# Performance work log

Hardware: AMD Instinct MI355X
Metric: run time of the kernel (lower is better)

Reference implementation:

```python
import jax, jax.numpy as jnp
import numpy as np

B, L, A, D = 16, 1024, 512, 1024


def setup_inputs() -> dict:
    key = jax.random.key(0)
    ks = jax.random.split(key, 12)
    s = 1.0 / np.sqrt(D)
    s2 = 1.0 / np.sqrt(2 * D)
    return {
        "text_features": jax.random.normal(ks[0], (B, L, D), jnp.float32),
        "audio_features": jax.random.normal(ks[1], (B, A, D), jnp.float32),
        "Wt1": jax.random.uniform(ks[2], (D, D), jnp.float32, -s, s),
        "bt1": jax.random.uniform(ks[3], (D,), jnp.float32, -s, s),
        "Wa1": jax.random.uniform(ks[4], (D, D), jnp.float32, -s, s),
        "w_att1": jax.random.uniform(ks[5], (2 * D,), jnp.float32, -s2, s2),
        "b_att1": jax.random.uniform(ks[6], (), jnp.float32, -s2, s2),
        "Wt2": jax.random.uniform(ks[7], (D, D), jnp.float32, -s, s),
        "Wa2": jax.random.uniform(ks[8], (D, D), jnp.float32, -s, s),
        "ba2": jax.random.uniform(ks[9], (D,), jnp.float32, -s, s),
        "w_att2": jax.random.uniform(ks[10], (2 * D,), jnp.float32, -s2, s2),
        "b_att2": jax.random.uniform(ks[11], (), jnp.float32, -s2, s2),
    }


def reference(text_features, audio_features, Wt1, bt1, Wa1, w_att1, b_att1,
              Wt2, Wa2, ba2, w_att2, b_att2):
    # Additive co-attention. tanh(cat([u_i, v_j])) = cat([tanh(u_i), tanh(v_j)]),
    # so the post-tanh linear score decomposes into an outer sum — exact same math
    # as the naive repeat/cat/tanh/linear, without the (B,L,A,2D) intermediate.
    d = Wt1.shape[0]
    # --- attention over audio regions ---
    u1 = jnp.tanh(jnp.einsum('bld,ed->ble', text_features, Wt1) + bt1)   # (B,L,D)
    v1 = jnp.tanh(jnp.einsum('bad,ed->bae', audio_features, Wa1))        # (B,A,D)
    scores1 = (u1 @ w_att1[:d])[:, :, None] + (v1 @ w_att1[d:])[:, None, :] + b_att1  # (B,L,A)
    audio_att = jax.nn.softmax(scores1, axis=-1)
    att_audio_features = jnp.einsum('bla,bad->bld', audio_att, audio_features)  # (B,L,D)
    # --- attention over text positions (self.args.max_seq_len == L) ---
    u2 = jnp.tanh(jnp.einsum('bld,ed->ble', att_audio_features, Wa2) + ba2)  # (B,L,D)
    v2 = jnp.tanh(jnp.einsum('bkd,ed->bke', text_features, Wt2))             # (B,L,D)
    scores2 = (u2 @ w_att2[:d])[:, :, None] + (v2 @ w_att2[d:])[:, None, :] + b_att2  # (B,L,L)
    textual_att = jax.nn.softmax(scores2, axis=-1)
    att_text_features = jnp.einsum('blk,bkd->bld', textual_att, text_features)
    return (att_text_features, att_audio_features)
```

## Files before the change

kernel.cpp:

```cpp
#include <hip/hip_runtime.h>

typedef unsigned short u16;
typedef float f32x4 __attribute__((ext_vector_type(4)));
typedef int   i32x4 __attribute__((ext_vector_type(4)));
typedef u16   u16x8 __attribute__((ext_vector_type(8)));

#define LDS_STRIDE 40

__device__ __forceinline__ u16 f2bf(float f) {
  unsigned u = __float_as_uint(f);
  u += 0x7FFFu + ((u >> 16) & 1u);
  return (u16)(u >> 16);
}

__device__ __forceinline__ float tanh_fast(float x) {
  float e = __expf(2.0f * x);
  return 1.0f - 2.0f / (e + 1.0f);
}

__device__ __forceinline__ void mfma_bf16(f32x4& acc, i32x4 a, i32x4 b) {
  asm("v_mfma_f32_16x16x32_bf16 %0, %1, %2, %0" : "+v"(acc) : "v"(a), "v"(b));
}

__global__ __launch_bounds__(256) void cast_all_kernel(
    const float* __restrict__ text, const float* __restrict__ audio,
    const float* __restrict__ w2, const float* __restrict__ w1,
    u16* __restrict__ tb, u16* __restrict__ ab,
    u16* __restrict__ w2b, u16* __restrict__ w1b) {
  const int NTOT = 3407872;
  int stride = gridDim.x * 256;
  for (int i = blockIdx.x * 256 + threadIdx.x; i < NTOT; i += stride) {
    const float* src; u16* dst; int j;
    if (i < 2097152)      { src = text;  dst = tb;  j = i; }
    else if (i < 3145728) { src = audio; dst = ab;  j = i - 2097152; }
    else if (i < 3276800) { src = w2;    dst = w2b; j = i - 3145728; }
    else                  { src = w1;    dst = w1b; j = i - 3276800; }
    const float4* s = (const float4*)src;
    float4 a = s[2 * j], b = s[2 * j + 1];
    u16x8 o;
    o[0] = f2bf(a.x); o[1] = f2bf(a.y); o[2] = f2bf(a.z); o[3] = f2bf(a.w);
    o[4] = f2bf(b.x); o[5] = f2bf(b.y); o[6] = f2bf(b.z); o[7] = f2bf(b.w);
    *(u16x8*)(dst + (size_t)8 * j) = o;
  }
}

__global__ __launch_bounds__(256) void score_kernel(
    const u16* __restrict__ Xa, const u16* __restrict__ Wa,
    const float* __restrict__ wva, float* __restrict__ sva,
    const u16* __restrict__ Xt, const u16* __restrict__ Wt,
    const float* __restrict__ wvt, float* __restrict__ svt) {
  __shared__ u16 At[128 * LDS_STRIDE];
  __shared__ u16 Bt[128 * LDS_STRIDE];

  int bx = blockIdx.x;
  const u16 *X, *W; const float* wv; float* svout; int mt, split, M;
  if (bx < 256) { X = Xa; W = Wa; wv = wva; svout = sva; M = 8192;  mt = bx >> 2; split = bx & 3; }
  else { bx -= 256; X = Xt; W = Wt; wv = wvt; svout = svt; M = 16384; mt = bx >> 2; split = bx & 3; }

  const int t = threadIdx.x;
  const int wid = t >> 6, lane = t & 63;
  const int wm = wid >> 1, wn = wid & 1;
  const int lane15 = lane & 15, lg = lane >> 4;
  const size_t m_base = (size_t)mt * 128;

  float rs[4][4];
  #pragma unroll
  for (int mi = 0; mi < 4; ++mi)
    #pragma unroll
    for (int r = 0; r < 4; ++r) rs[mi][r] = 0.f;

  const int li0 = t, li1 = 256 + t;
  const int ar0 = li0 >> 2, ac0 = (li0 & 3) * 8;
  const int ar1 = li1 >> 2, ac1 = (li1 & 3) * 8;

  for (int nt = 0; nt < 2; ++nt) {
    const int n0 = split * 256 + nt * 128;

    f32x4 acc[4][4];
    #pragma unroll
    for (int mi = 0; mi < 4; ++mi)
      #pragma unroll
      for (int ni = 0; ni < 4; ++ni)
        acc[mi][ni] = (f32x4){0.f, 0.f, 0.f, 0.f};

    const u16* Xb = X + m_base * 1024;
    const u16* Wb = W + (size_t)n0 * 1024;

    i32x4 ra0 = *(const i32x4*)(Xb + (size_t)ar0 * 1024 + ac0);
    i32x4 ra1 = *(const i32x4*)(Xb + (size_t)ar1 * 1024 + ac1);
    i32x4 rb0 = *(const i32x4*)(Wb + (size_t)ar0 * 1024 + ac0);
    i32x4 rb1 = *(const i32x4*)(Wb + (size_t)ar1 * 1024 + ac1);

    for (int kt = 0; kt < 32; ++kt) {
      __syncthreads();
      *(i32x4*)(At + li0 * 8 / 8 * 0 + ar0 * LDS_STRIDE + ac0) = ra0;
      *(i32x4*)(At + ar1 * LDS_STRIDE + ac1) = ra1;
      *(i32x4*)(Bt + ar0 * LDS_STRIDE + ac0) = rb0;
      *(i32x4*)(Bt + ar1 * LDS_STRIDE + ac1) = rb1;
      __syncthreads();
      if (kt < 31) {
        const int k1 = (kt + 1) * 32;
        ra0 = *(const i32x4*)(Xb + (size_t)ar0 * 1024 + k1 + ac0);
        ra1 = *(const i32x4*)(Xb + (size_t)ar1 * 1024 + k1 + ac1);
        rb0 = *(const i32x4*)(Wb + (size_t)ar0 * 1024 + k1 + ac0);
        rb1 = *(const i32x4*)(Wb + (size_t)ar1 * 1024 + k1 + ac1);
      }
      i32x4 af[4], bfr[4];
      #pragma unroll
      for (int mi = 0; mi < 4; ++mi)
        af[mi] = *(const i32x4*)(At + (wm * 64 + mi * 16 + lane15) * LDS_STRIDE + lg * 8);
      #pragma unroll
      for (int ni = 0; ni < 4; ++ni)
        bfr[ni] = *(const i32x4*)(Bt + (wn * 64 + ni * 16 + lane15) * LDS_STRIDE + lg * 8);
      #pragma unroll
      for (int mi = 0; mi < 4; ++mi)
        #pragma unroll
        for (int ni = 0; ni < 4; ++ni)
          mfma_bf16(acc[mi][ni], af[mi], bfr[ni]);
    }

    float wvn[4];
    #pragma unroll
    for (int ni = 0; ni < 4; ++ni) wvn[ni] = wv[n0 + wn * 64 + ni * 16 + lane15];
    #pragma unroll
    for (int mi = 0; mi < 4; ++mi)
      #pragma unroll
      for (int ni = 0; ni < 4; ++ni)
        #pragma unroll
        for (int r = 0; r < 4; ++r)
          rs[mi][r] += tanh_fast(acc[mi][ni][r]) * wvn[ni];
  }

  __syncthreads();
  float* sred = (float*)At;
  #pragma unroll
  for (int mi = 0; mi < 4; ++mi)
    #pragma unroll
    for (int r = 0; r < 4; ++r) {
      float v = rs[mi][r];
      v += __shfl_xor(v, 1);
      v += __shfl_xor(v, 2);
      v += __shfl_xor(v, 4);
      v += __shfl_xor(v, 8);
      if (lane15 == 0) sred[wn * 128 + wm * 64 + mi * 16 + lg * 4 + r] = v;
    }
  __syncthreads();
  if (t < 128) svout[(size_t)split * M + m_base + t] = sred[t] + sred[128 + t];
}

__global__ __launch_bounds__(256) void softq_bcast_kernel(
    const float* __restrict__ xA, const float* __restrict__ svA,
    const float* __restrict__ xT, const float* __restrict__ svT,
    float* __restrict__ out) {
  int bx = blockIdx.x;
  int stage = bx >> 8;
  int b = (bx >> 4) & 15, dch = bx & 15;
  int Acnt = stage ? 1024 : 512;
  int M = stage ? 16384 : 8192;
  const float* x = stage ? xT : xA;
  const float* svp = stage ? svT : svA;
  int rowbase = b * Acnt;

  __shared__ float p[1024];
  __shared__ float red[256];
  __shared__ float chunk[64];
  int t = threadIdx.x;

  float mloc = -1e30f;
  for (int a = t; a < Acnt; a += 256) {
    float v = svp[rowbase + a] + svp[M + rowbase + a] +
              svp[2 * M + rowbase + a] + svp[3 * M + rowbase + a];
    p[a] = v;
    mloc = fmaxf(mloc, v);
  }
  #pragma unroll
  for (int off = 32; off; off >>= 1) mloc = fmaxf(mloc, __shfl_xor(mloc, off));
  if ((t & 63) == 0) red[t >> 6] = mloc;
  __syncthreads();
  float mx = fmaxf(fmaxf(red[0], red[1]), fmaxf(red[2], red[3]));

  float sloc = 0.f;
  for (int a = t; a < Acnt; a += 256) {
    float e = __expf(p[a] - mx);
    p[a] = e;
    sloc += e;
  }
  #pragma unroll
  for (int off = 32; off; off >>= 1) sloc += __shfl_xor(sloc, off);
  __syncthreads();
  if ((t & 63) == 0) red[t >> 6] = sloc;
  __syncthreads();
  float inv = 1.0f / (red[0] + red[1] + red[2] + red[3]);

  int dl = t & 63, ag = t >> 6;
  const float* xb = x + (size_t)rowbase * 1024 + dch * 64 + dl;
  float acc = 0.f;
  #pragma unroll 4
  for (int a = ag; a < Acnt; a += 4) acc += p[a] * xb[(size_t)a * 1024];
  __syncthreads();
  red[t] = acc;
  __syncthreads();
  if (t < 64) {
    float tot = red[t] + red[t + 64] + red[t + 128] + red[t + 192];
    chunk[t] = tot * inv;
  }
  __syncthreads();

  size_t base4 = ((stage ? (size_t)0 : (size_t)16777216) +
                  (size_t)b * 1048576 + (size_t)dch * 64) >> 2;
  float4* o4 = (float4*)out;
  float4 v = ((float4*)chunk)[t & 15];
  int q = t & 15;
  #pragma unroll 4
  for (int l = t >> 4; l < 1024; l += 16)
    o4[base4 + (size_t)l * 256 + q] = v;
}

extern "C" void kernel_launch(void* const* d_in, const int* in_sizes, int n_in,
                              void* d_out, int out_size, void* d_ws, size_t ws_size,
                              hipStream_t stream) {
  const float* text  = (const float*)d_in[0];
  const float* audio = (const float*)d_in[1];
  const float* Wa1   = (const float*)d_in[4];
  const float* watt1 = (const float*)d_in[5];
  const float* Wt2   = (const float*)d_in[7];
  const float* watt2 = (const float*)d_in[10];

  char* ws = (char*)d_ws;
  u16*   tb  = (u16*)(ws);
  u16*   ab  = (u16*)(ws + 33554432);
  u16*   w2b = (u16*)(ws + 50331648);
  u16*   w1b = (u16*)(ws + 52428800);
  float* sv2 = (float*)(ws + 54525952);
  float* sv1 = (float*)(ws + 54788096);

  cast_all_kernel<<<2048, 256, 0, stream>>>(text, audio, Wt2, Wa1, tb, ab, w2b, w1b);

  score_kernel<<<768, 256, 0, stream>>>(ab, w1b, watt1 + 1024, sv1,
                                        tb, w2b, watt2 + 1024, sv2);

  softq_bcast_kernel<<<512, 256, 0, stream>>>(audio, sv1, text, sv2, (float*)d_out);
}
```

Measured before the change: 349.3 us.

## Fuse activation bf16 cast into score GEMM, swizzle LDS, nontemporal broadcast stores

The separate cast pass over text and audio activations is removed. The score GEMM now loads fp32 activations directly and converts them to bf16 in registers with packed cvt before writing to LDS, so a full bf16 copy of the inputs is no longer written and re-read. LDS padding is replaced by an XOR swizzle, the block-to-tile mapping is remapped so blocks sharing a weight slice run together, the softmax reduction loop is unrolled further, and output broadcast stores use nontemporal hints. In exchange, the GEMM A-operand loads become twice as wide in bytes, and each activation tile is cast once per n-tile and per split instead of once overall.

```diff
diff --git a/kernel.cpp b/kernel.cpp
--- a/kernel.cpp
+++ b/kernel.cpp
@@ -5,7 +5,7 @@
 typedef int   i32x4 __attribute__((ext_vector_type(4)));
 typedef u16   u16x8 __attribute__((ext_vector_type(8)));
 
-#define LDS_STRIDE 40
+#define SWZ(i) ((i) ^ ((((i) >> 6) & 3) << 3))
 
 __device__ __forceinline__ u16 f2bf(float f) {
   unsigned u = __float_as_uint(f);
@@ -13,6 +13,12 @@
   return (u16)(u >> 16);
 }
 
+__device__ __forceinline__ int cvt_pk_bf16(float lo, float hi) {
+  int r;
+  asm("v_cvt_pk_bf16_f32 %0, %1, %2" : "=v"(r) : "v"(lo), "v"(hi));
+  return r;
+}
+
 __device__ __forceinline__ float tanh_fast(float x) {
   float e = __expf(2.0f * x);
   return 1.0f - 2.0f / (e + 1.0f);
@@ -22,40 +28,39 @@
   asm("v_mfma_f32_16x16x32_bf16 %0, %1, %2, %0" : "+v"(acc) : "v"(a), "v"(b));
 }
 
-__global__ __launch_bounds__(256) void cast_all_kernel(
-    const float* __restrict__ text, const float* __restrict__ audio,
+__global__ __launch_bounds__(256) void wcast_kernel(
     const float* __restrict__ w2, const float* __restrict__ w1,
-    u16* __restrict__ tb, u16* __restrict__ ab,
     u16* __restrict__ w2b, u16* __restrict__ w1b) {
-  const int NTOT = 3407872;
-  int stride = gridDim.x * 256;
-  for (int i = blockIdx.x * 256 + threadIdx.x; i < NTOT; i += stride) {
-    const float* src; u16* dst; int j;
-    if (i < 2097152)      { src = text;  dst = tb;  j = i; }
-    else if (i < 3145728) { src = audio; dst = ab;  j = i - 2097152; }
-    else if (i < 3276800) { src = w2;    dst = w2b; j = i - 3145728; }
-    else                  { src = w1;    dst = w1b; j = i - 3276800; }
-    const float4* s = (const float4*)src;
-    float4 a = s[2 * j], b = s[2 * j + 1];
-    u16x8 o;
-    o[0] = f2bf(a.x); o[1] = f2bf(a.y); o[2] = f2bf(a.z); o[3] = f2bf(a.w);
-    o[4] = f2bf(b.x); o[5] = f2bf(b.y); o[6] = f2bf(b.z); o[7] = f2bf(b.w);
-    *(u16x8*)(dst + (size_t)8 * j) = o;
-  }
+  int i = blockIdx.x * 256 + threadIdx.x;
+  const float* src; u16* dst; int j;
+  if (i < 131072) { src = w2; dst = w2b; j = i; }
+  else            { src = w1; dst = w1b; j = i - 131072; }
+  const float4* s = (const float4*)src;
+  float4 a = s[2 * j], b = s[2 * j + 1];
+  u16x8 o;
+  o[0] = f2bf(a.x); o[1] = f2bf(a.y); o[2] = f2bf(a.z); o[3] = f2bf(a.w);
+  o[4] = f2bf(b.x); o[5] = f2bf(b.y); o[6] = f2bf(b.z); o[7] = f2bf(b.w);
+  *(u16x8*)(dst + (size_t)8 * j) = o;
 }
 
 __global__ __launch_bounds__(256) void score_kernel(
-    const u16* __restrict__ Xa, const u16* __restrict__ Wa,
+    const float* __restrict__ audio, const u16* __restrict__ w1b,
     const float* __restrict__ wva, float* __restrict__ sva,
-    const u16* __restrict__ Xt, const u16* __restrict__ Wt,
+    const float* __restrict__ text, const u16* __restrict__ w2b,
     const float* __restrict__ wvt, float* __restrict__ svt) {
-  __shared__ u16 At[128 * LDS_STRIDE];
-  __shared__ u16 Bt[128 * LDS_STRIDE];
+  __shared__ u16 At[128 * 32];
+  __shared__ u16 Bt[128 * 32];
 
   int bx = blockIdx.x;
-  const u16 *X, *W; const float* wv; float* svout; int mt, split, M;
-  if (bx < 256) { X = Xa; W = Wa; wv = wva; svout = sva; M = 8192;  mt = bx >> 2; split = bx & 3; }
-  else { bx -= 256; X = Xt; W = Wt; wv = wvt; svout = svt; M = 16384; mt = bx >> 2; split = bx & 3; }
+  const float* Xf; const u16* Wb_; const float* wv; float* svout; int mt, split, M;
+  if (bx < 256) {
+    Xf = audio; Wb_ = w1b; wv = wva; svout = sva; M = 8192;
+    mt = (bx & 7) * 8 + (bx >> 5); split = (bx >> 3) & 3;
+  } else {
+    int x = bx - 256;
+    Xf = text; Wb_ = w2b; wv = wvt; svout = svt; M = 16384;
+    mt = (x & 7) * 16 + (x >> 5); split = (x >> 3) & 3;
+  }
 
   const int t = threadIdx.x;
   const int wid = t >> 6, lane = t & 63;
@@ -69,9 +74,11 @@
     #pragma unroll
     for (int r = 0; r < 4; ++r) rs[mi][r] = 0.f;
 
-  const int li0 = t, li1 = 256 + t;
-  const int ar0 = li0 >> 2, ac0 = (li0 & 3) * 8;
-  const int ar1 = li1 >> 2, ac1 = (li1 & 3) * 8;
+  const int ar0 = t >> 2,        ac0 = (t & 3) * 8;
+  const int ar1 = (256 + t) >> 2, ac1 = (t & 3) * 8;
+  const int wiA0 = SWZ(ar0 * 32 + ac0), wiA1 = SWZ(ar1 * 32 + ac1);
+
+  const float* Xb = Xf + m_base * 1024;
 
   for (int nt = 0; nt < 2; ++nt) {
     const int n0 = split * 256 + nt * 128;
@@ -83,35 +90,47 @@
       for (int ni = 0; ni < 4; ++ni)
         acc[mi][ni] = (f32x4){0.f, 0.f, 0.f, 0.f};
 
-    const u16* Xb = X + m_base * 1024;
-    const u16* Wb = W + (size_t)n0 * 1024;
-
-    i32x4 ra0 = *(const i32x4*)(Xb + (size_t)ar0 * 1024 + ac0);
-    i32x4 ra1 = *(const i32x4*)(Xb + (size_t)ar1 * 1024 + ac1);
-    i32x4 rb0 = *(const i32x4*)(Wb + (size_t)ar0 * 1024 + ac0);
-    i32x4 rb1 = *(const i32x4*)(Wb + (size_t)ar1 * 1024 + ac1);
+    const u16* Wp = Wb_ + (size_t)n0 * 1024;
+
+    float4 xa0 = *(const float4*)(Xb + (size_t)ar0 * 1024 + ac0);
+    float4 xa0b = *(const float4*)(Xb + (size_t)ar0 * 1024 + ac0 + 4);
+    float4 xa1 = *(const float4*)(Xb + (size_t)ar1 * 1024 + ac1);
+    float4 xa1b = *(const float4*)(Xb + (size_t)ar1 * 1024 + ac1 + 4);
+    i32x4 rb0 = *(const i32x4*)(Wp + (size_t)ar0 * 1024 + ac0);
+    i32x4 rb1 = *(const i32x4*)(Wp + (size_t)ar1 * 1024 + ac1);
 
     for (int kt = 0; kt < 32; ++kt) {
+      i32x4 wa0, wa1;
+      wa0[0] = cvt_pk_bf16(xa0.x, xa0.y);  wa0[1] = cvt_pk_bf16(xa0.z, xa0.w);
+      wa0[2] = cvt_pk_bf16(xa0b.x, xa0b.y); wa0[3] = cvt_pk_bf16(xa0b.z, xa0b.w);
+      wa1[0] = cvt_pk_bf16(xa1.x, xa1.y);  wa1[1] = cvt_pk_bf16(xa1.z, xa1.w);
+      wa1[2] = cvt_pk_bf16(xa1b.x, xa1b.y); wa1[3] = cvt_pk_bf16(xa1b.z, xa1b.w);
       __syncthreads();
-      *(i32x4*)(At + li0 * 8 / 8 * 0 + ar0 * LDS_STRIDE + ac0) = ra0;
-      *(i32x4*)(At + ar1 * LDS_STRIDE + ac1) = ra1;
-      *(i32x4*)(Bt + ar0 * LDS_STRIDE + ac0) = rb0;
-      *(i32x4*)(Bt + ar1 * LDS_STRIDE + ac1) = rb1;
+      *(i32x4*)(At + wiA0) = wa0;
+      *(i32x4*)(At + wiA1) = wa1;
+      *(i32x4*)(Bt + wiA0) = rb0;
+      *(i32x4*)(Bt + wiA1) = rb1;
       __syncthreads();
       if (kt < 31) {
         const int k1 = (kt + 1) * 32;
-        ra0 = *(const i32x4*)(Xb + (size_t)ar0 * 1024 + k1 + ac0);
-        ra1 = *(const i32x4*)(Xb + (size_t)ar1 * 1024 + k1 + ac1);
-        rb0 = *(const i32x4*)(Wb + (size_t)ar0 * 1024 + k1 + ac0);
-        rb1 = *(const i32x4*)(Wb + (size_t)ar1 * 1024 + k1 + ac1);
+        xa0  = *(const float4*)(Xb + (size_t)ar0 * 1024 + k1 + ac0);
+        xa0b = *(const float4*)(Xb + (size_t)ar0 * 1024 + k1 + ac0 + 4);
+        xa1  = *(const float4*)(Xb + (size_t)ar1 * 1024 + k1 + ac1);
+        xa1b = *(const float4*)(Xb + (size_t)ar1 * 1024 + k1 + ac1 + 4);
+        rb0  = *(const i32x4*)(Wp + (size_t)ar0 * 1024 + k1 + ac0);
+        rb1  = *(const i32x4*)(Wp + (size_t)ar1 * 1024 + k1 + ac1);
       }
       i32x4 af[4], bfr[4];
       #pragma unroll
-      for (int mi = 0; mi < 4; ++mi)
-        af[mi] = *(const i32x4*)(At + (wm * 64 + mi * 16 + lane15) * LDS_STRIDE + lg * 8);
-      #pragma unroll
-      for (int ni = 0; ni < 4; ++ni)
-        bfr[ni] = *(const i32x4*)(Bt + (wn * 64 + ni * 16 + lane15) * LDS_STRIDE + lg * 8);
+      for (int mi = 0; mi < 4; ++mi) {
+        int rr = wm * 64 + mi * 16 + lane15;
+        af[mi] = *(const i32x4*)(At + SWZ(rr * 32 + lg * 8));
+      }
+      #pragma unroll
+      for (int ni = 0; ni < 4; ++ni) {
+        int rr = wn * 64 + ni * 16 + lane15;
+        bfr[ni] = *(const i32x4*)(Bt + SWZ(rr * 32 + lg * 8));
+      }
       #pragma unroll
       for (int mi = 0; mi < 4; ++mi)
         #pragma unroll
@@ -195,7 +214,7 @@
   int dl = t & 63, ag = t >> 6;
   const float* xb = x + (size_t)rowbase * 1024 + dch * 64 + dl;
   float acc = 0.f;
-  #pragma unroll 4
+  #pragma unroll 8
   for (int a = ag; a < Acnt; a += 4) acc += p[a] * xb[(size_t)a * 1024];
   __syncthreads();
   red[t] = acc;
@@ -208,12 +227,12 @@
 
   size_t base4 = ((stage ? (size_t)0 : (size_t)16777216) +
                   (size_t)b * 1048576 + (size_t)dch * 64) >> 2;
-  float4* o4 = (float4*)out;
-  float4 v = ((float4*)chunk)[t & 15];
+  f32x4* o4 = (f32x4*)out;
+  f32x4 v = ((f32x4*)chunk)[t & 15];
   int q = t & 15;
   #pragma unroll 4
   for (int l = t >> 4; l < 1024; l += 16)
-    o4[base4 + (size_t)l * 256 + q] = v;
+    __builtin_nontemporal_store(v, &o4[base4 + (size_t)l * 256 + q]);
 }
 
 extern "C" void kernel_launch(void* const* d_in, const int* in_sizes, int n_in,
@@ -227,17 +246,15 @@
   const float* watt2 = (const float*)d_in[10];
 
   char* ws = (char*)d_ws;
-  u16*   tb  = (u16*)(ws);
-  u16*   ab  = (u16*)(ws + 33554432);
-  u16*   w2b = (u16*)(ws + 50331648);
-  u16*   w1b = (u16*)(ws + 52428800);
-  float* sv2 = (float*)(ws + 54525952);
-  float* sv1 = (float*)(ws + 54788096);
-
-  cast_all_kernel<<<2048, 256, 0, stream>>>(text, audio, Wt2, Wa1, tb, ab, w2b, w1b);
-
-  score_kernel<<<768, 256, 0, stream>>>(ab, w1b, watt1 + 1024, sv1,
-                                        tb, w2b, watt2 + 1024, sv2);
+  u16*   w2b = (u16*)(ws);
+  u16*   w1b = (u16*)(ws + 2097152);
+  float* sv2 = (float*)(ws + 4194304);
+  float* sv1 = (float*)(ws + 4456448);
+
+  wcast_kernel<<<1024, 256, 0, stream>>>(Wt2, Wa1, w2b, w1b);
+
+  score_kernel<<<768, 256, 0, stream>>>(audio, w1b, watt1 + 1024, sv1,
+                                        text, w2b, watt2 + 1024, sv2);
 
   softq_bcast_kernel<<<512, 256, 0, stream>>>(audio, sv1, text, sv2, (float*)d_out);
 }
```

New measurement: 352.9 us. Within noise of the previous version (+1.0%).

## Restructure score GEMM with 512-thread 128x256 tiles, double-buffered swizzled LDS

Applied to the files above, without the earlier changes.

The score GEMM kernel now uses 512 threads per block. Each block computes a full 128x256 output tile in one pass instead of two sequential 128x128 passes. The LDS is double-buffered and XOR-swizzled rather than padded, which halves the barriers per k-step and overlaps the next tile's store with compute. The block-index mapping is remapped to group M tiles for better L2 reuse of weights. The softmax/broadcast kernel gets a deeper unroll and nontemporal stores for the large broadcast output, at the cost of higher register and LDS pressure per block.

```diff
diff --git a/kernel.cpp b/kernel.cpp
--- a/kernel.cpp
+++ b/kernel.cpp
@@ -5,7 +5,7 @@
 typedef int   i32x4 __attribute__((ext_vector_type(4)));
 typedef u16   u16x8 __attribute__((ext_vector_type(8)));
 
-#define LDS_STRIDE 40
+#define SWZ(i) ((i) ^ ((((i) >> 6) & 3) << 3))
 
 __device__ __forceinline__ u16 f2bf(float f) {
   unsigned u = __float_as_uint(f);
@@ -44,94 +44,100 @@
   }
 }
 
-__global__ __launch_bounds__(256) void score_kernel(
+__global__ __launch_bounds__(512, 4) void score_kernel(
     const u16* __restrict__ Xa, const u16* __restrict__ Wa,
     const float* __restrict__ wva, float* __restrict__ sva,
     const u16* __restrict__ Xt, const u16* __restrict__ Wt,
     const float* __restrict__ wvt, float* __restrict__ svt) {
-  __shared__ u16 At[128 * LDS_STRIDE];
-  __shared__ u16 Bt[128 * LDS_STRIDE];
+  __shared__ u16 At[2][4096];
+  __shared__ u16 Bt[2][8192];
 
   int bx = blockIdx.x;
   const u16 *X, *W; const float* wv; float* svout; int mt, split, M;
-  if (bx < 256) { X = Xa; W = Wa; wv = wva; svout = sva; M = 8192;  mt = bx >> 2; split = bx & 3; }
-  else { bx -= 256; X = Xt; W = Wt; wv = wvt; svout = svt; M = 16384; mt = bx >> 2; split = bx & 3; }
+  if (bx < 256) {
+    X = Xa; W = Wa; wv = wva; svout = sva; M = 8192;
+    mt = (bx >> 5) * 8 + (bx & 7); split = (bx >> 3) & 3;
+  } else {
+    int x = bx - 256;
+    X = Xt; W = Wt; wv = wvt; svout = svt; M = 16384;
+    mt = (x >> 5) * 8 + (x & 7); split = (x >> 3) & 3;
+  }
+  const int n0 = split * 256;
 
   const int t = threadIdx.x;
   const int wid = t >> 6, lane = t & 63;
-  const int wm = wid >> 1, wn = wid & 1;
+  const int wm = wid >> 2, wn = wid & 3;
   const int lane15 = lane & 15, lg = lane >> 4;
-  const size_t m_base = (size_t)mt * 128;
-
-  float rs[4][4];
+
+  const int sr = t >> 2, sc = (t & 3) * 8;
+  const int wiA  = SWZ(sr * 32 + sc);
+  const int wiB1 = SWZ((128 + sr) * 32 + sc);
+
+  const u16* Xb = X + (size_t)mt * 128 * 1024;
+  const u16* Wp = W + (size_t)n0 * 1024;
+
+  f32x4 acc[4][4];
   #pragma unroll
   for (int mi = 0; mi < 4; ++mi)
     #pragma unroll
-    for (int r = 0; r < 4; ++r) rs[mi][r] = 0.f;
-
-  const int li0 = t, li1 = 256 + t;
-  const int ar0 = li0 >> 2, ac0 = (li0 & 3) * 8;
-  const int ar1 = li1 >> 2, ac1 = (li1 & 3) * 8;
-
-  for (int nt = 0; nt < 2; ++nt) {
-    const int n0 = split * 256 + nt * 128;
-
-    f32x4 acc[4][4];
+    for (int ni = 0; ni < 4; ++ni)
+      acc[mi][ni] = (f32x4){0.f, 0.f, 0.f, 0.f};
+
+  i32x4 ra  = *(const i32x4*)(Xb + (size_t)sr * 1024 + sc);
+  i32x4 rb0 = *(const i32x4*)(Wp + (size_t)sr * 1024 + sc);
+  i32x4 rb1 = *(const i32x4*)(Wp + (size_t)(128 + sr) * 1024 + sc);
+  *(i32x4*)(At[0] + wiA)  = ra;
+  *(i32x4*)(Bt[0] + wiA)  = rb0;
+  *(i32x4*)(Bt[0] + wiB1) = rb1;
+  __syncthreads();
+
+  for (int kt = 0; kt < 32; ++kt) {
+    const int cur = kt & 1;
+    if (kt < 31) {
+      const int k1 = (kt + 1) * 32;
+      ra  = *(const i32x4*)(Xb + (size_t)sr * 1024 + k1 + sc);
+      rb0 = *(const i32x4*)(Wp + (size_t)sr * 1024 + k1 + sc);
+      rb1 = *(const i32x4*)(Wp + (size_t)(128 + sr) * 1024 + k1 + sc);
+    }
+    i32x4 af[4], bfr[4];
+    #pragma unroll
+    for (int mi = 0; mi < 4; ++mi) {
+      int rr = wm * 64 + mi * 16 + lane15;
+      af[mi] = *(const i32x4*)(At[cur] + SWZ(rr * 32 + lg * 8));
+    }
+    #pragma unroll
+    for (int ni = 0; ni < 4; ++ni) {
+      int rr = wn * 64 + ni * 16 + lane15;
+      bfr[ni] = *(const i32x4*)(Bt[cur] + SWZ(rr * 32 + lg * 8));
+    }
     #pragma unroll
     for (int mi = 0; mi < 4; ++mi)
       #pragma unroll
       for (int ni = 0; ni < 4; ++ni)
-        acc[mi][ni] = (f32x4){0.f, 0.f, 0.f, 0.f};
-
-    const u16* Xb = X + m_base * 1024;
-    const u16* Wb = W + (size_t)n0 * 1024;
-
-    i32x4 ra0 = *(const i32x4*)(Xb + (size_t)ar0 * 1024 + ac0);
-    i32x4 ra1 = *(const i32x4*)(Xb + (size_t)ar1 * 1024 + ac1);
-    i32x4 rb0 = *(const i32x4*)(Wb + (size_t)ar0 * 1024 + ac0);
-    i32x4 rb1 = *(const i32x4*)(Wb + (size_t)ar1 * 1024 + ac1);
-
-    for (int kt = 0; kt < 32; ++kt) {
-      __syncthreads();
-      *(i32x4*)(At + li0 * 8 / 8 * 0 + ar0 * LDS_STRIDE + ac0) = ra0;
-      *(i32x4*)(At + ar1 * LDS_STRIDE + ac1) = ra1;
-      *(i32x4*)(Bt + ar0 * LDS_STRIDE + ac0) = rb0;
-      *(i32x4*)(Bt + ar1 * LDS_STRIDE + ac1) = rb1;
-      __syncthreads();
-      if (kt < 31) {
-        const int k1 = (kt + 1) * 32;
-        ra0 = *(const i32x4*)(Xb + (size_t)ar0 * 1024 + k1 + ac0);
-        ra1 = *(const i32x4*)(Xb + (size_t)ar1 * 1024 + k1 + ac1);
-        rb0 = *(const i32x4*)(Wb + (size_t)ar0 * 1024 + k1 + ac0);
-        rb1 = *(const i32x4*)(Wb + (size_t)ar1 * 1024 + k1 + ac1);
-      }
-      i32x4 af[4], bfr[4];
-      #pragma unroll
-      for (int mi = 0; mi < 4; ++mi)
-        af[mi] = *(const i32x4*)(At + (wm * 64 + mi * 16 + lane15) * LDS_STRIDE + lg * 8);
+        mfma_bf16(acc[mi][ni], af[mi], bfr[ni]);
+    if (kt < 31) {
+      *(i32x4*)(At[cur ^ 1] + wiA)  = ra;
+      *(i32x4*)(Bt[cur ^ 1] + wiA)  = rb0;
+      *(i32x4*)(Bt[cur ^ 1] + wiB1) = rb1;
+    }
+    __syncthreads();
+  }
+
+  float wvn[4];
+  #pragma unroll
+  for (int ni = 0; ni < 4; ++ni) wvn[ni] = wv[n0 + wn * 64 + ni * 16 + lane15];
+  float rs[4][4];
+  #pragma unroll
+  for (int mi = 0; mi < 4; ++mi)
+    #pragma unroll
+    for (int r = 0; r < 4; ++r) {
+      float v = 0.f;
       #pragma unroll
       for (int ni = 0; ni < 4; ++ni)
-        bfr[ni] = *(const i32x4*)(Bt + (wn * 64 + ni * 16 + lane15) * LDS_STRIDE + lg * 8);
-      #pragma unroll
-      for (int mi = 0; mi < 4; ++mi)
-        #pragma unroll
-        for (int ni = 0; ni < 4; ++ni)
-          mfma_bf16(acc[mi][ni], af[mi], bfr[ni]);
-    }
-
-    float wvn[4];
-    #pragma unroll
-    for (int ni = 0; ni < 4; ++ni) wvn[ni] = wv[n0 + wn * 64 + ni * 16 + lane15];
-    #pragma unroll
-    for (int mi = 0; mi < 4; ++mi)
-      #pragma unroll
-      for (int ni = 0; ni < 4; ++ni)
-        #pragma unroll
-        for (int r = 0; r < 4; ++r)
-          rs[mi][r] += tanh_fast(acc[mi][ni][r]) * wvn[ni];
-  }
-
-  __syncthreads();
+        v += tanh_fast(acc[mi][ni][r]) * wvn[ni];
+      rs[mi][r] = v;
+    }
+
   float* sred = (float*)At;
   #pragma unroll
   for (int mi = 0; mi < 4; ++mi)
@@ -142,10 +148,13 @@
       v += __shfl_xor(v, 2);
       v += __shfl_xor(v, 4);
       v += __shfl_xor(v, 8);
-      if (lane15 == 0) sred[wn * 128 + wm * 64 + mi * 16 + lg * 4 + r] = v;
-    }
-  __syncthreads();
-  if (t < 128) svout[(size_t)split * M + m_base + t] = sred[t] + sred[128 + t];
+      if (lane15 == 0)
+        sred[wn * 128 + wm * 64 + mi * 16 + lg * 4 + r] = v;
+    }
+  __syncthreads();
+  if (t < 128)
+    svout[(size_t)split * M + (size_t)mt * 128 + t] =
+        sred[t] + sred[128 + t] + sred[256 + t] + sred[384 + t];
 }
 
 __global__ __launch_bounds__(256) void softq_bcast_kernel(
@@ -195,7 +204,7 @@
   int dl = t & 63, ag = t >> 6;
   const float* xb = x + (size_t)rowbase * 1024 + dch * 64 + dl;
   float acc = 0.f;
-  #pragma unroll 4
+  #pragma unroll 8
   for (int a = ag; a < Acnt; a += 4) acc += p[a] * xb[(size_t)a * 1024];
   __syncthreads();
   red[t] = acc;
@@ -208,12 +217,12 @@
 
   size_t base4 = ((stage ? (size_t)0 : (size_t)16777216) +
                   (size_t)b * 1048576 + (size_t)dch * 64) >> 2;
-  float4* o4 = (float4*)out;
-  float4 v = ((float4*)chunk)[t & 15];
+  f32x4* o4 = (f32x4*)out;
+  f32x4 v = ((f32x4*)chunk)[t & 15];
   int q = t & 15;
   #pragma unroll 4
   for (int l = t >> 4; l < 1024; l += 16)
-    o4[base4 + (size_t)l * 256 + q] = v;
+    __builtin_nontemporal_store(v, &o4[base4 + (size_t)l * 256 + q]);
 }
 
 extern "C" void kernel_launch(void* const* d_in, const int* in_sizes, int n_in,
@@ -234,10 +243,12 @@
   float* sv2 = (float*)(ws + 54525952);
   float* sv1 = (float*)(ws + 54788096);
 
-  cast_all_kernel<<<2048, 256, 0, stream>>>(text, audio, Wt2, Wa1, tb, ab, w2b, w1b);
-
-  score_kernel<<<768, 256, 0, stream>>>(ab, w1b, watt1 + 1024, sv1,
+  cast_all_kernel<<<2048, 256, 0, stream>>>(text, audio, Wt2, Wa1,
+                                            tb, ab, w2b, w1b);
+
+  score_kernel<<<768, 512, 0, stream>>>(ab, w1b, watt1 + 1024, sv1,
                                         tb, w2b, watt2 + 1024, sv2);
 
-  softq_bcast_kernel<<<512, 256, 0, stream>>>(audio, sv1, text, sv2, (float*)d_out);
-}
+  softq_bcast_kernel<<<512, 256, 0, stream>>>(audio, sv1, text, sv2,
+                                              (float*)d_out);
+}
```

Measured after the change: 323.7 us. 1.08x faster.
